# Kernel tuning notes

Measured on AMD Instinct MI355X. Metric: run time of the kernel, lower is better.

Reference implementation:

```python
import jax, jax.numpy as jnp
import numpy as np

B, N, D_IN = 16, 2048, 256
C, H = 32, 64          # num_capsules, dim_capsules
HEADS, KD = 4, 64      # attention heads, key_dim = dim_capsules
ROUTINGS = 3
EPS_SQ = 1e-7
LN_EPS = 1e-3


def squash(v, axis=-1):
    s2 = jnp.sum(jnp.square(v), axis=axis, keepdims=True)
    scale = s2 / (1.0 + s2) / jnp.sqrt(s2 + EPS_SQ)
    return scale * v


def setup_inputs() -> dict:
    key = jax.random.key(0)
    ks = jax.random.split(key, 10)
    # VarianceScaling(scale=2.0, fan_avg, uniform) for W
    fan_avg = (D_IN + H) / 2.0
    limit = float(np.sqrt(3.0 * 2.0 / fan_avg))
    W = jax.random.uniform(ks[0], (C, D_IN, H), minval=-limit, maxval=limit, dtype=jnp.float32)
    b_caps = jnp.zeros((C, H), jnp.float32)
    gamma = jnp.full((1,), 3.0, jnp.float32)
    x = jax.random.normal(ks[1], (B, N, D_IN), dtype=jnp.float32)
    def glorot(k, shape):
        fin, fout = shape[0], int(np.prod(shape[1:]))
        lim = float(np.sqrt(6.0 / (fin + fout)))
        return jax.random.uniform(k, shape, minval=-lim, maxval=lim, dtype=jnp.float32)
    Wq = glorot(ks[2], (H, HEADS, KD)); bq = jnp.zeros((HEADS, KD), jnp.float32)
    Wk = glorot(ks[3], (H, HEADS, KD)); bk = jnp.zeros((HEADS, KD), jnp.float32)
    Wv = glorot(ks[4], (H, HEADS, KD)); bv = jnp.zeros((HEADS, KD), jnp.float32)
    Wo = glorot(ks[5], (HEADS, KD, H)); bo = jnp.zeros((H,), jnp.float32)
    ln_gamma = jnp.ones((H,), jnp.float32)
    ln_beta = jnp.zeros((H,), jnp.float32)
    return dict(x=x, W=W, b_caps=b_caps, gamma=gamma,
                Wq=Wq, bq=bq, Wk=Wk, bk=bk, Wv=Wv, bv=bv, Wo=Wo, bo=bo,
                ln_gamma=ln_gamma, ln_beta=ln_beta)


def dynamic_routing(u_hat):
    # u_hat: [B, N, C, H]
    b = jnp.zeros(u_hat.shape[:3] + (1,), u_hat.dtype)
    v = None
    for i in range(ROUTINGS):
        c = jax.nn.softmax(b, axis=2)                      # [B,N,C,1]
        s = jnp.sum(c * u_hat, axis=1, keepdims=True)      # [B,1,C,H]
        v = squash(s, axis=-1)
        if i < ROUTINGS - 1:
            agreement = jnp.sum(u_hat * v, axis=-1, keepdims=True)
            b = b + agreement
    return jnp.squeeze(v, axis=1)                          # [B,C,H]


def mha_self(xq, Wq, bq, Wk, bk, Wv, bv, Wo, bo):
    # xq: [B, C, H]
    q = jnp.einsum('bch,hnk->bcnk', xq, Wq) + bq
    k = jnp.einsum('bch,hnk->bcnk', xq, Wk) + bk
    v = jnp.einsum('bch,hnk->bcnk', xq, Wv) + bv
    scores = jnp.einsum('bqnd,bknd->bnqk', q, k) / jnp.sqrt(jnp.asarray(KD, xq.dtype))
    attn = jax.nn.softmax(scores, axis=-1)
    ctx = jnp.einsum('bnqk,bknd->bqnd', attn, v)
    return jnp.einsum('bqnd,ndh->bqh', ctx, Wo) + bo


def reference(x, W, b_caps, gamma, Wq, bq, Wk, bk, Wv, bv, Wo, bo, ln_gamma, ln_beta):
    u_hat = jnp.einsum('bnd,cdh->bnch', x, W) + b_caps[None, None]  # [B,N,C,H]
    routed = dynamic_routing(u_hat)                                  # [B,C,H]
    attended = mha_self(routed, Wq, bq, Wk, bk, Wv, bv, Wo, bo)
    y = attended + routed
    mu = jnp.mean(y, axis=-1, keepdims=True)
    var = jnp.mean(jnp.square(y - mu), axis=-1, keepdims=True)
    routed = (y - mu) / jnp.sqrt(var + LN_EPS) * ln_gamma + ln_beta
    return squash(routed, axis=-1) * gamma
```

## Files before the change

### kernel.cpp

```cpp
#include <hip/hip_runtime.h>
#include <hip/hip_cooperative_groups.h>
#include <cstddef>

namespace cg = cooperative_groups;

typedef _Float16 f16;
typedef __attribute__((ext_vector_type(8))) _Float16 f16x8;
typedef __attribute__((ext_vector_type(4))) float f32x4;

namespace {
constexpr int kB = 16;
constexpr int kN = 2048;
constexpr int kD = 256;
constexpr int kC = 32;
constexpr int kH = 64;
constexpr int kHeads = 4;
constexpr int kKD = 64;
constexpr int kChunks = 32;
constexpr int kRows = kN / kChunks;
constexpr int kXJ = 64;

constexpr size_t OFF_XPART = 0;
constexpr size_t OFF_V     = OFF_XPART + 262144;
constexpr size_t OFF_WV    = OFF_V + 32768;
constexpr size_t OFF_BV    = OFF_WV + 131072;
constexpr size_t OFF_Y     = OFF_BV + 512;
constexpr size_t OFF_CS    = OFF_Y + 131072;
constexpr size_t OFF_QKV   = OFF_CS + 512;
constexpr size_t OFF_CTX   = OFF_QKV + 393216;
constexpr size_t OFF_XF16  = OFF_CTX + 524288;
constexpr size_t OFF_WVH   = OFF_XF16 + 4194304;
constexpr size_t OFF_CSP   = OFF_WVH + 65536;
constexpr size_t OFF_YP    = OFF_CSP + 16384;
constexpr size_t WS_NEED_PARTIAL = (OFF_YP + 4194304) * sizeof(float);

struct SMemR {
  f16 xsT[kD][kRows + 8];
  float aL[kRows][kC + 4];
  f16 pT[kC][kRows + 8];
  float csL[8][kC];
  float yL[kD];
  float sL[4][kH];
  float vL[kH];
  float csLs;
};
struct SMemA {
  float rL[kC * kH];
  float qL[kC][kKD];
  float kL[kC][kKD + 1];
  float vL[kC][kKD];
  float sc[kC][kC + 1];
};
struct SMemF {
  float cL[kHeads * kKD];
  float sL[4][kH];
};
union SMemU { SMemR r; SMemA a; SMemF f; };
}


template <int CW, int ACC, int WRV>
__device__ __forceinline__ void sv_tail(const float* __restrict__ W,
                                        const float* __restrict__ b_caps,
                                        SMemR& r, float* __restrict__ v,
                                        float* __restrict__ Wv, f16* __restrict__ wvh,
                                        float* __restrict__ bv, int b, int c, int t) {
  const int w = t >> 6, h = t & 63;
  const float* Wc = W + (size_t)c * kD * kH;
  {
    float acc = 0.f;
#pragma unroll 8
    for (int d = w * 64; d < (w + 1) * 64; ++d)
      acc = fmaf(r.yL[d], Wc[(size_t)d * kH + h], acc);
    r.sL[w][h] = acc;
  }
  __syncthreads();
  if (t < 64) {
    const float bch = b_caps[c * kH + h];
    float s = r.sL[0][h] + r.sL[1][h] + r.sL[2][h] + r.sL[3][h] + r.csLs * bch;
    float s2 = s * s;
#pragma unroll
    for (int off = 32; off; off >>= 1) s2 += __shfl_xor(s2, off, 64);
    const float scale = s2 / (1.f + s2) * rsqrtf(s2 + 1e-7f);
    const float vh = scale * s;
    if (WRV) v[((size_t)b * kC + c) * kH + h] = vh;
    r.vL[h] = vh;
    if (CW) {
      float bvp = bch * vh;
#pragma unroll
      for (int off = 32; off; off >>= 1) bvp += __shfl_xor(bvp, off, 64);
      if (h == 0) bv[b * kC + c] = ACC ? (bv[b * kC + c] + bvp) : bvp;
    }
  }
  __syncthreads();
  if (CW) {
    float acc = 0.f;
    const float* Wrow = Wc + (size_t)t * kH;
#pragma unroll 8
    for (int hh = 0; hh < kH; ++hh) acc = fmaf(Wrow[hh], r.vL[hh], acc);
    const size_t idx = ((size_t)b * kC + c) * kD + t;
    const float nv = ACC ? (Wv[idx] + acc) : acc;
    Wv[idx] = nv;
    wvh[idx] = (f16)nv;
  }
}

__device__ __forceinline__ void route_phase(SMemR& r, const f16x8* __restrict__ af,
                                            const f16* __restrict__ wvh,
                                            const float* __restrict__ bv,
                                            f16* __restrict__ yp, float* __restrict__ csp,
                                            int b, int chunk, int t) {
  const int lane = t & 63, w = t >> 6;
  const int l15 = lane & 15, q = lane >> 4;
  const float bvc = bv[b * kC + (t & 31)];

  f32x4 acc0 = {0.f, 0.f, 0.f, 0.f}, acc1 = {0.f, 0.f, 0.f, 0.f};
  {
    const f16x8* B0 = reinterpret_cast<const f16x8*>(
        wvh + ((size_t)(b * kC + l15)) * kD + q * 8);
    const f16x8* B1 = reinterpret_cast<const f16x8*>(
        wvh + ((size_t)(b * kC + 16 + l15)) * kD + q * 8);
#pragma unroll
    for (int ks = 0; ks < 8; ++ks) {
      acc0 = __builtin_amdgcn_mfma_f32_16x16x32_f16(af[ks], B0[ks * 4], acc0, 0, 0, 0);
      acc1 = __builtin_amdgcn_mfma_f32_16x16x32_f16(af[ks], B1[ks * 4], acc1, 0, 0, 0);
    }
  }
#pragma unroll
  for (int rr = 0; rr < 4; ++rr) {
    r.aL[w * 16 + q * 4 + rr][l15] = acc0[rr];
    r.aL[w * 16 + q * 4 + rr][16 + l15] = acc1[rr];
  }
  __syncthreads();

  const int c = t & 31, sg = t >> 5;
  float csreg = 0.f;
#pragma unroll
  for (int k = 0; k < 8; ++k) {
    const int rr = sg * 8 + k;
    float L = bvc + r.aL[rr][c];
    float m = L;
#pragma unroll
    for (int off = 16; off; off >>= 1) m = fmaxf(m, __shfl_xor(m, off, 64));
    const float e = __expf(L - m);
    float ssum = e;
#pragma unroll
    for (int off = 16; off; off >>= 1) ssum += __shfl_xor(ssum, off, 64);
    const float p = e / ssum;
    r.pT[c][rr] = (f16)p;
    csreg += p;
  }
  r.csL[sg][c] = csreg;
  __syncthreads();

  const int mt2 = w & 1;
  const int ntb = (w >> 1) * 8;
  const f16x8 a0 = *reinterpret_cast<const f16x8*>(&r.pT[mt2 * 16 + l15][q * 8]);
  const f16x8 a1 = *reinterpret_cast<const f16x8*>(&r.pT[mt2 * 16 + l15][32 + q * 8]);
  const int cap = mt2 * 16 + q * 4;
#pragma unroll
  for (int i = 0; i < 8; ++i) {
    const int d0 = (ntb + i) * 16;
    const f16x8 b0 = *reinterpret_cast<const f16x8*>(&r.xsT[d0 + l15][q * 8]);
    const f16x8 b1 = *reinterpret_cast<const f16x8*>(&r.xsT[d0 + l15][32 + q * 8]);
    f32x4 o = {0.f, 0.f, 0.f, 0.f};
    o = __builtin_amdgcn_mfma_f32_16x16x32_f16(a0, b0, o, 0, 0, 0);
    o = __builtin_amdgcn_mfma_f32_16x16x32_f16(a1, b1, o, 0, 0, 0);
    f16* dst = yp + (((size_t)(b * kChunks + chunk)) * kC + cap) * kD + d0 + l15;
#pragma unroll
    for (int rr = 0; rr < 4; ++rr) dst[(size_t)rr * kD] = (f16)o[rr];
  }
  if (t < 32) {
    float s = 0.f;
#pragma unroll
    for (int j = 0; j < 8; ++j) s += r.csL[j][t];
    csp[((size_t)b * kChunks + chunk) * kC + t] = s;
  }
}

__global__ __launch_bounds__(256, 2) void k_fused(
    const float* __restrict__ x, const float* __restrict__ W,
    const float* __restrict__ b_caps, const float* __restrict__ gamma,
    const float* __restrict__ Wq, const float* __restrict__ bq,
    const float* __restrict__ Wk, const float* __restrict__ bk,
    const float* __restrict__ Wvp, const float* __restrict__ bvp,
    const float* __restrict__ Wo, const float* __restrict__ bo,
    const float* __restrict__ ln_g, const float* __restrict__ ln_b,
    float* __restrict__ out, float* __restrict__ ws) {
  float* xpart = ws + OFF_XPART;
  float* v     = ws + OFF_V;
  float* Wv    = ws + OFF_WV;
  float* bv    = ws + OFF_BV;
  float* ctx   = ws + OFF_CTX;
  f16*   wvh   = (f16*)(ws + OFF_WVH);
  float* csp   = ws + OFF_CSP;
  f16*   yp    = (f16*)(ws + OFF_YP);

  const int b = blockIdx.x, chunk = blockIdx.y;
  const int t = threadIdx.x;
  const int lane = t & 63, w = t >> 6;
  const int l15 = lane & 15, q = lane >> 4;
  const int n0 = chunk * kRows;
  const int c = chunk;

  __shared__ __align__(16) SMemU sm;
  cg::grid_group grid = cg::this_grid();

  {
    const float* xc = x + ((size_t)b * kN + n0) * kD + t;
    float s = 0.f;
#pragma unroll 16
    for (int n = 0; n < kRows; ++n) s += xc[(size_t)n * kD];
    xpart[((size_t)b * kChunks + chunk) * kD + t] = s;
  }
  f16x8 af[8];
  {
    const int row = w * 16 + l15;
    const float* xr = x + ((size_t)(b * kN + n0 + row)) * kD + q * 8;
#pragma unroll
    for (int ks = 0; ks < 8; ++ks) {
      const f32x4* p = reinterpret_cast<const f32x4*>(xr + ks * 32);
      const f32x4 lo = p[0], hi = p[1];
      f16x8 a;
      a[0] = (f16)lo[0]; a[1] = (f16)lo[1]; a[2] = (f16)lo[2]; a[3] = (f16)lo[3];
      a[4] = (f16)hi[0]; a[5] = (f16)hi[1]; a[6] = (f16)hi[2]; a[7] = (f16)hi[3];
      af[ks] = a;
      const int dbase = ks * 32 + q * 8;
#pragma unroll
      for (int i = 0; i < 8; ++i) {
        const int ii = (i + 2 * q) & 7;
        sm.r.xsT[dbase + ii][row] = a[ii];
      }
    }
  }
  grid.sync();

  {
    float s = 0.f;
#pragma unroll 8
    for (int ch = 0; ch < kChunks; ++ch)
      s += xpart[((size_t)b * kChunks + ch) * kD + t];
    sm.r.yL[t] = s * (1.f / (float)kC);
    if (t == 0) sm.r.csLs = (float)kN / (float)kC;
  }
  __syncthreads();
  sv_tail<1, 0, 0>(W, b_caps, sm.r, v, Wv, wvh, bv, b, c, t);
  grid.sync();

  route_phase(sm.r, af, wvh, bv, yp, csp, b, chunk, t);
  grid.sync();

  {
    float s = 0.f;
#pragma unroll 8
    for (int ch = 0; ch < kChunks; ++ch)
      s += (float)yp[(((size_t)b * kChunks + ch) * kC + c) * kD + t];
    sm.r.yL[t] = s;
    if (t < 32) {
      float cs_ = csp[((size_t)b * kChunks + t) * kC + c];
#pragma unroll
      for (int off = 16; off; off >>= 1) cs_ += __shfl_xor(cs_, off, 64);
      if (t == 0) sm.r.csLs = cs_;
    }
  }
  __syncthreads();
  sv_tail<1, 1, 0>(W, b_caps, sm.r, v, Wv, wvh, bv, b, c, t);
  grid.sync();

  route_phase(sm.r, af, wvh, bv, yp, csp, b, chunk, t);
  grid.sync();

  {
    float s = 0.f;
#pragma unroll 8
    for (int ch = 0; ch < kChunks; ++ch)
      s += (float)yp[(((size_t)b * kChunks + ch) * kC + c) * kD + t];
    sm.r.yL[t] = s;
    if (t < 32) {
      float cs_ = csp[((size_t)b * kChunks + t) * kC + c];
#pragma unroll
      for (int off = 16; off; off >>= 1) cs_ += __shfl_xor(cs_, off, 64);
      if (t == 0) sm.r.csLs = cs_;
    }
  }
  __syncthreads();
  sv_tail<0, 0, 1>(W, b_caps, sm.r, v, Wv, wvh, bv, b, c, t);
  grid.sync();

  if (chunk < kHeads) {
    const int head = chunk;
    const int kk = t & 63;
#pragma unroll
    for (int i = 0; i < 8; ++i)
      sm.a.rL[t + 256 * i] = v[(size_t)b * kC * kH + t + 256 * i];
    __syncthreads();
    float aq[8], ak[8], av[8];
    const float bbq = bq[head * kKD + kk];
    const float bbk = bk[head * kKD + kk];
    const float bbv = bvp[head * kKD + kk];
#pragma unroll
    for (int i = 0; i < 8; ++i) { aq[i] = bbq; ak[i] = bbk; av[i] = bbv; }
#pragma unroll 4
    for (int hh = 0; hh < kH; ++hh) {
      const size_t widx = ((size_t)hh * kHeads + head) * kKD + kk;
      const float wq = Wq[widx];
      const float wk2 = Wk[widx];
      const float wv2 = Wvp[widx];
#pragma unroll
      for (int i = 0; i < 8; ++i) {
        const float rv = sm.a.rL[(w + 4 * i) * kH + hh];
        aq[i] = fmaf(rv, wq, aq[i]);
        ak[i] = fmaf(rv, wk2, ak[i]);
        av[i] = fmaf(rv, wv2, av[i]);
      }
    }
#pragma unroll
    for (int i = 0; i < 8; ++i) {
      const int cc = w + 4 * i;
      sm.a.qL[cc][kk] = aq[i];
      sm.a.kL[cc][kk] = ak[i];
      sm.a.vL[cc][kk] = av[i];
    }
    __syncthreads();
#pragma unroll
    for (int i = 0; i < 4; ++i) {
      const int e = t + 256 * i, qc = e >> 5, kc2 = e & 31;
      float s = 0.f;
#pragma unroll 8
      for (int d = 0; d < kKD; ++d) s = fmaf(sm.a.qL[qc][d], sm.a.kL[kc2][d], s);
      sm.a.sc[qc][kc2] = s * 0.125f;
    }
    __syncthreads();
    if (t < kC) {
      float m = -1e30f;
#pragma unroll
      for (int kc2 = 0; kc2 < kC; ++kc2) m = fmaxf(m, sm.a.sc[t][kc2]);
      float ssum = 0.f;
#pragma unroll
      for (int kc2 = 0; kc2 < kC; ++kc2) {
        const float e2 = __expf(sm.a.sc[t][kc2] - m);
        sm.a.sc[t][kc2] = e2;
        ssum += e2;
      }
      const float inv = 1.f / ssum;
#pragma unroll
      for (int kc2 = 0; kc2 < kC; ++kc2) sm.a.sc[t][kc2] *= inv;
    }
    __syncthreads();
#pragma unroll
    for (int i = 0; i < 8; ++i) {
      const int e = t + 256 * i, qc = e >> 6, d = e & 63;
      float s = 0.f;
#pragma unroll 8
      for (int kc2 = 0; kc2 < kC; ++kc2) s = fmaf(sm.a.sc[qc][kc2], sm.a.vL[kc2][d], s);
      ctx[(((size_t)b * kC + qc) * kHeads + head) * kKD + d] = s;
    }
  }
  grid.sync();

  {
    const int bc = b * kC + chunk;
    const int h = t & 63;
    sm.f.cL[t] = ctx[(size_t)bc * (kHeads * kKD) + t];
    __syncthreads();
    float acc = 0.f;
#pragma unroll 8
    for (int nd = w * 64; nd < (w + 1) * 64; ++nd)
      acc = fmaf(sm.f.cL[nd], Wo[(size_t)nd * kH + h], acc);
    sm.f.sL[w][h] = acc;
    __syncthreads();
    if (t < 64) {
      const float yv = sm.f.sL[0][h] + sm.f.sL[1][h] + sm.f.sL[2][h] + sm.f.sL[3][h] +
                       bo[h] + v[(size_t)bc * kH + h];
      float mu = yv;
#pragma unroll
      for (int off = 32; off; off >>= 1) mu += __shfl_xor(mu, off, 64);
      mu *= (1.f / (float)kH);
      const float dv = yv - mu;
      float var = dv * dv;
#pragma unroll
      for (int off = 32; off; off >>= 1) var += __shfl_xor(var, off, 64);
      var *= (1.f / (float)kH);
      const float nrm = dv * rsqrtf(var + 1e-3f) * ln_g[h] + ln_b[h];
      float s2 = nrm * nrm;
#pragma unroll
      for (int off = 32; off; off >>= 1) s2 += __shfl_xor(s2, off, 64);
      const float scale = s2 / (1.f + s2) * rsqrtf(s2 + 1e-7f);
      out[(size_t)bc * kH + h] = scale * nrm * gamma[0];
    }
  }
}


__global__ __launch_bounds__(256) void k_xpart(const float* __restrict__ x,
                                               float* __restrict__ xpart,
                                               f16* __restrict__ xh) {
  const int b = blockIdx.x, j = blockIdx.y, d = threadIdx.x;
  const size_t base = ((size_t)b * kN + (size_t)j * 32) * kD + d;
  const float* xp = x + base;
  f16* xo = xh + base;
  float s = 0.f;
#pragma unroll
  for (int n = 0; n < 32; ++n) {
    const float v = xp[(size_t)n * kD];
    s += v;
    xo[(size_t)n * kD] = (f16)v;
  }
  xpart[((size_t)b * kXJ + j) * kD + d] = s;
}

__global__ __launch_bounds__(256) void k_sv(
    const float* __restrict__ W, const float* __restrict__ b_caps,
    const float* __restrict__ xpart, const float* __restrict__ y,
    const float* __restrict__ csum, const f16* __restrict__ ypart,
    const float* __restrict__ cspart, float* __restrict__ v,
    float* __restrict__ Wv, f16* __restrict__ Wvh, float* __restrict__ bv,
    const int mode, const int computeWv, const int accWv, const int npart) {
  const int bc = blockIdx.x, b = bc >> 5, c = bc & 31;
  const int t = threadIdx.x;
  const int w = t >> 6, h = t & 63;
  __shared__ float yL[kD];
  __shared__ float sL[4][kH];
  __shared__ float vL[kH];
  __shared__ float csLs;

  if (mode == 0) {
    float s = 0.f;
#pragma unroll 8
    for (int j = 0; j < kXJ; ++j) s += xpart[((size_t)b * kXJ + j) * kD + t];
    yL[t] = s * (1.f / (float)kC);
    if (t == 0) csLs = (float)kN / (float)kC;
  } else if (npart > 0) {
    float s = 0.f;
#pragma unroll 8
    for (int ch = 0; ch < kChunks; ++ch)
      s += (float)ypart[(((size_t)b * kChunks + ch) * kC + c) * kD + t];
    yL[t] = s;
    if (t < 32) {
      float cs_ = cspart[((size_t)b * kChunks + t) * kC + c];
#pragma unroll
      for (int off = 16; off; off >>= 1) cs_ += __shfl_xor(cs_, off, 64);
      if (t == 0) csLs = cs_;
    }
  } else {
    yL[t] = y[(size_t)bc * kD + t];
    if (t == 0) csLs = csum[bc];
  }
  __syncthreads();

  const float* Wc = W + (size_t)c * kD * kH;
  {
    float acc = 0.f;
#pragma unroll 8
    for (int d = w * 64; d < (w + 1) * 64; ++d)
      acc = fmaf(yL[d], Wc[(size_t)d * kH + h], acc);
    sL[w][h] = acc;
  }
  __syncthreads();

  if (t < 64) {
    const float bch = b_caps[c * kH + h];
    float s = sL[0][h] + sL[1][h] + sL[2][h] + sL[3][h] + csLs * bch;
    float s2 = s * s;
#pragma unroll
    for (int off = 32; off; off >>= 1) s2 += __shfl_xor(s2, off, 64);
    const float scale = s2 / (1.f + s2) * rsqrtf(s2 + 1e-7f);
    const float vh = scale * s;
    v[(size_t)bc * kH + h] = vh;
    vL[h] = vh;
    if (computeWv) {
      float bvp = bch * vh;
#pragma unroll
      for (int off = 32; off; off >>= 1) bvp += __shfl_xor(bvp, off, 64);
      if (h == 0) bv[bc] = accWv ? (bv[bc] + bvp) : bvp;
    }
  }
  __syncthreads();
  if (computeWv) {
    float acc = 0.f;
    const float* Wrow = Wc + (size_t)t * kH;
#pragma unroll 8
    for (int hh = 0; hh < kH; ++hh) acc = fmaf(Wrow[hh], vL[hh], acc);
    const size_t idx = (size_t)bc * kD + t;
    const float nv = accWv ? (Wv[idx] + acc) : acc;
    Wv[idx] = nv;
    Wvh[idx] = (f16)nv;
  }
}

__global__ __launch_bounds__(256) void k_route(
    const f16* __restrict__ xh, const f16* __restrict__ Wvh,
    const float* __restrict__ bv, float* __restrict__ y,
    float* __restrict__ csum, f16* __restrict__ ypart,
    float* __restrict__ cspart, const int usePart) {
  const int b = blockIdx.x, chunk = blockIdx.y;
  const int t = threadIdx.x;
  const int lane = t & 63, w = t >> 6;
  const int l15 = lane & 15, q = lane >> 4;

  __shared__ __align__(16) f16 xsT[kD][kRows + 8];
  __shared__ float aL[kRows][kC + 4];
  __shared__ __align__(16) f16 pT[kC][kRows + 8];
  __shared__ float csL[8][kC];

  const int n0 = chunk * kRows;
  const float bvc = bv[b * kC + (t & 31)];

  f32x4 acc0 = {0.f, 0.f, 0.f, 0.f}, acc1 = {0.f, 0.f, 0.f, 0.f};
  {
    const int row = w * 16 + l15;
    const f16x8* Ar = reinterpret_cast<const f16x8*>(
        xh + ((size_t)(b * kN + n0 + row)) * kD + q * 8);
    const f16x8* B0 = reinterpret_cast<const f16x8*>(
        Wvh + ((size_t)(b * kC + l15)) * kD + q * 8);
    const f16x8* B1 = reinterpret_cast<const f16x8*>(
        Wvh + ((size_t)(b * kC + 16 + l15)) * kD + q * 8);
#pragma unroll
    for (int ks = 0; ks < 8; ++ks) {
      f16x8 af = Ar[ks * 4];
      acc0 = __builtin_amdgcn_mfma_f32_16x16x32_f16(af, B0[ks * 4], acc0, 0, 0, 0);
      acc1 = __builtin_amdgcn_mfma_f32_16x16x32_f16(af, B1[ks * 4], acc1, 0, 0, 0);
      const int dbase = ks * 32 + q * 8;
#pragma unroll
      for (int i = 0; i < 8; ++i) {
        const int ii = (i + 2 * q) & 7;
        xsT[dbase + ii][row] = af[ii];
      }
    }
  }
#pragma unroll
  for (int r = 0; r < 4; ++r) {
    aL[w * 16 + q * 4 + r][l15] = acc0[r];
    aL[w * 16 + q * 4 + r][16 + l15] = acc1[r];
  }
  __syncthreads();

  const int c = t & 31, sg = t >> 5;
  float csreg = 0.f;
#pragma unroll
  for (int k = 0; k < 8; ++k) {
    const int r = sg * 8 + k;
    float L = bvc + aL[r][c];
    float m = L;
#pragma unroll
    for (int off = 16; off; off >>= 1) m = fmaxf(m, __shfl_xor(m, off, 64));
    const float e = __expf(L - m);
    float ssum = e;
#pragma unroll
    for (int off = 16; off; off >>= 1) ssum += __shfl_xor(ssum, off, 64);
    const float p = e / ssum;
    pT[c][r] = (f16)p;
    csreg += p;
  }
  csL[sg][c] = csreg;
  __syncthreads();

  const int mt2 = w & 1;
  const int ntb = (w >> 1) * 8;
  const f16x8 a0 = *reinterpret_cast<const f16x8*>(&pT[mt2 * 16 + l15][q * 8]);
  const f16x8 a1 = *reinterpret_cast<const f16x8*>(&pT[mt2 * 16 + l15][32 + q * 8]);
  const int cap = mt2 * 16 + q * 4;
#pragma unroll
  for (int i = 0; i < 8; ++i) {
    const int d0 = (ntb + i) * 16;
    const f16x8 b0 = *reinterpret_cast<const f16x8*>(&xsT[d0 + l15][q * 8]);
    const f16x8 b1 = *reinterpret_cast<const f16x8*>(&xsT[d0 + l15][32 + q * 8]);
    f32x4 o = {0.f, 0.f, 0.f, 0.f};
    o = __builtin_amdgcn_mfma_f32_16x16x32_f16(a0, b0, o, 0, 0, 0);
    o = __builtin_amdgcn_mfma_f32_16x16x32_f16(a1, b1, o, 0, 0, 0);
    if (usePart) {
      f16* dst = ypart + (((size_t)(b * kChunks + chunk)) * kC + cap) * kD + d0 + l15;
#pragma unroll
      for (int r = 0; r < 4; ++r) dst[(size_t)r * kD] = (f16)o[r];
    } else {
      float* dst = y + ((size_t)(b * kC + cap)) * kD + d0 + l15;
#pragma unroll
      for (int r = 0; r < 4; ++r) atomicAdd(dst + (size_t)r * kD, o[r]);
    }
  }
  if (t < 32) {
    float s = 0.f;
#pragma unroll
    for (int j = 0; j < 8; ++j) s += csL[j][t];
    if (usePart) cspart[((size_t)b * kChunks + chunk) * kC + t] = s;
    else atomicAdd(csum + b * kC + t, s);
  }
}

__global__ __launch_bounds__(256) void k_attn(
    const float* __restrict__ routed,
    const float* __restrict__ Wq, const float* __restrict__ bq,
    const float* __restrict__ Wk, const float* __restrict__ bk,
    const float* __restrict__ Wvp, const float* __restrict__ bvp,
    float* __restrict__ ctx) {
  const int b = blockIdx.x, head = blockIdx.y, t = threadIdx.x;
  const int kk = t & 63, w = t >> 6;
  __shared__ float rL[kC * kH];
  __shared__ float qL[kC][kKD];
  __shared__ float kL[kC][kKD + 1];
  __shared__ float vL[kC][kKD];
  __shared__ float sc[kC][kC + 1];
#pragma unroll
  for (int i = 0; i < 8; ++i) rL[t + 256 * i] = routed[(size_t)b * kC * kH + t + 256 * i];
  __syncthreads();
  float aq[8], ak[8], av[8];
  const float bbq = bq[head * kKD + kk];
  const float bbk = bk[head * kKD + kk];
  const float bbv = bvp[head * kKD + kk];
#pragma unroll
  for (int i = 0; i < 8; ++i) { aq[i] = bbq; ak[i] = bbk; av[i] = bbv; }
#pragma unroll 4
  for (int hh = 0; hh < kH; ++hh) {
    const size_t widx = ((size_t)hh * kHeads + head) * kKD + kk;
    const float wq = Wq[widx];
    const float wk2 = Wk[widx];
    const float wv2 = Wvp[widx];
#pragma unroll
    for (int i = 0; i < 8; ++i) {
      const float r = rL[(w + 4 * i) * kH + hh];
      aq[i] = fmaf(r, wq, aq[i]);
      ak[i] = fmaf(r, wk2, ak[i]);
      av[i] = fmaf(r, wv2, av[i]);
    }
  }
#pragma unroll
  for (int i = 0; i < 8; ++i) {
    const int cc = w + 4 * i;
    qL[cc][kk] = aq[i];
    kL[cc][kk] = ak[i];
    vL[cc][kk] = av[i];
  }
  __syncthreads();
#pragma unroll
  for (int i = 0; i < 4; ++i) {
    const int e = t + 256 * i, qc = e >> 5, kc2 = e & 31;
    float s = 0.f;
#pragma unroll 8
    for (int d = 0; d < kKD; ++d) s = fmaf(qL[qc][d], kL[kc2][d], s);
    sc[qc][kc2] = s * 0.125f;
  }
  __syncthreads();
  if (t < kC) {
    float m = -1e30f;
#pragma unroll
    for (int kc2 = 0; kc2 < kC; ++kc2) m = fmaxf(m, sc[t][kc2]);
    float ssum = 0.f;
#pragma unroll
    for (int kc2 = 0; kc2 < kC; ++kc2) {
      const float e2 = __expf(sc[t][kc2] - m);
      sc[t][kc2] = e2;
      ssum += e2;
    }
    const float inv = 1.f / ssum;
#pragma unroll
    for (int kc2 = 0; kc2 < kC; ++kc2) sc[t][kc2] *= inv;
  }
  __syncthreads();
#pragma unroll
  for (int i = 0; i < 8; ++i) {
    const int e = t + 256 * i, qc = e >> 6, d = e & 63;
    float s = 0.f;
#pragma unroll 8
    for (int kc2 = 0; kc2 < kC; ++kc2) s = fmaf(sc[qc][kc2], vL[kc2][d], s);
    ctx[(((size_t)b * kC + qc) * kHeads + head) * kKD + d] = s;
  }
}

__global__ __launch_bounds__(256) void k_final(
    const float* __restrict__ ctx, const float* __restrict__ Wo,
    const float* __restrict__ bo, const float* __restrict__ routed,
    const float* __restrict__ ln_g, const float* __restrict__ ln_b,
    const float* __restrict__ gamma, float* __restrict__ out) {
  const int bc = blockIdx.x, t = threadIdx.x;
  const int w = t >> 6, h = t & 63;
  __shared__ float cL[kHeads * kKD];
  __shared__ float sL[4][kH];
  cL[t] = ctx[(size_t)bc * (kHeads * kKD) + t];
  __syncthreads();
  float acc = 0.f;
#pragma unroll 8
  for (int nd = w * 64; nd < (w + 1) * 64; ++nd)
    acc = fmaf(cL[nd], Wo[(size_t)nd * kH + h], acc);
  sL[w][h] = acc;
  __syncthreads();
  if (t < 64) {
    const float yv = sL[0][h] + sL[1][h] + sL[2][h] + sL[3][h] + bo[h] +
                     routed[(size_t)bc * kH + h];
    float mu = yv;
#pragma unroll
    for (int off = 32; off; off >>= 1) mu += __shfl_xor(mu, off, 64);
    mu *= (1.f / (float)kH);
    const float dv = yv - mu;
    float var = dv * dv;
#pragma unroll
    for (int off = 32; off; off >>= 1) var += __shfl_xor(var, off, 64);
    var *= (1.f / (float)kH);
    const float nrm = dv * rsqrtf(var + 1e-3f) * ln_g[h] + ln_b[h];
    float s2 = nrm * nrm;
#pragma unroll
    for (int off = 32; off; off >>= 1) s2 += __shfl_xor(s2, off, 64);
    const float scale = s2 / (1.f + s2) * rsqrtf(s2 + 1e-7f);
    out[(size_t)bc * kH + h] = scale * nrm * gamma[0];
  }
}

extern "C" void kernel_launch(void* const* d_in, const int* in_sizes, int n_in,
                              void* d_out, int out_size, void* d_ws, size_t ws_size,
                              hipStream_t stream) {
  (void)in_sizes; (void)n_in; (void)out_size;
  const float* x      = (const float*)d_in[0];
  const float* W      = (const float*)d_in[1];
  const float* b_caps = (const float*)d_in[2];
  const float* gamma  = (const float*)d_in[3];
  const float* Wq     = (const float*)d_in[4];
  const float* bq     = (const float*)d_in[5];
  const float* Wk     = (const float*)d_in[6];
  const float* bk     = (const float*)d_in[7];
  const float* Wv_in  = (const float*)d_in[8];
  const float* bv_in  = (const float*)d_in[9];
  const float* Wo     = (const float*)d_in[10];
  const float* bo     = (const float*)d_in[11];
  const float* ln_g   = (const float*)d_in[12];
  const float* ln_b   = (const float*)d_in[13];
  float* out = (float*)d_out;
  float* ws  = (float*)d_ws;

  static int s_coop = -1;
  if (s_coop < 0) {
    int dev = 0;
    hipGetDevice(&dev);
    hipDeviceProp_t prop{};
    hipGetDeviceProperties(&prop, dev);
    int occ = 0;
    hipError_t e = hipOccupancyMaxActiveBlocksPerMultiprocessor(&occ, k_fused, 256, 0);
    s_coop = (e == hipSuccess && prop.cooperativeLaunch &&
              (long long)occ * prop.multiProcessorCount >= (long long)kB * kChunks)
                 ? 1 : 0;
  }

  if (s_coop && ws_size >= WS_NEED_PARTIAL) {
    void* args[] = {(void*)&x,     (void*)&W,     (void*)&b_caps, (void*)&gamma,
                    (void*)&Wq,    (void*)&bq,    (void*)&Wk,     (void*)&bk,
                    (void*)&Wv_in, (void*)&bv_in, (void*)&Wo,     (void*)&bo,
                    (void*)&ln_g,  (void*)&ln_b,  (void*)&out,    (void*)&ws};
    hipLaunchCooperativeKernel((void*)k_fused, dim3(kB, kChunks), dim3(256, 1, 1),
                               args, 0, stream);
    return;
  }

  float* xpart = ws + OFF_XPART;
  float* v     = ws + OFF_V;
  float* Wv    = ws + OFF_WV;
  float* bv    = ws + OFF_BV;
  float* y     = ws + OFF_Y;
  float* cs    = ws + OFF_CS;
  float* ctx   = ws + OFF_CTX;
  f16*   xf16  = (f16*)(ws + OFF_XF16);
  f16*   wvh   = (f16*)(ws + OFF_WVH);
  float* csp   = ws + OFF_CSP;
  f16*   yp    = (f16*)(ws + OFF_YP);

  const int usePart = (ws_size >= WS_NEED_PARTIAL) ? 1 : 0;

  k_xpart<<<dim3(kB, kXJ), 256, 0, stream>>>(x, xpart, xf16);
  k_sv<<<kB * kC, 256, 0, stream>>>(W, b_caps, xpart, y, cs, yp, csp, v, Wv, wvh, bv,
                                    0, 1, 0, 0);
  if (!usePart) {
    hipMemsetAsync(y, 0, (size_t)kB * kC * kD * sizeof(float), stream);
    hipMemsetAsync(cs, 0, (size_t)kB * kC * sizeof(float), stream);
  }
  k_route<<<dim3(kB, kChunks), 256, 0, stream>>>(xf16, wvh, bv, y, cs, yp, csp, usePart);
  k_sv<<<kB * kC, 256, 0, stream>>>(W, b_caps, xpart, y, cs, yp, csp, v, Wv, wvh, bv,
                                    1, 1, 1, usePart ? kChunks : 0);
  if (!usePart) {
    hipMemsetAsync(y, 0, (size_t)kB * kC * kD * sizeof(float), stream);
    hipMemsetAsync(cs, 0, (size_t)kB * kC * sizeof(float), stream);
  }
  k_route<<<dim3(kB, kChunks), 256, 0, stream>>>(xf16, wvh, bv, y, cs, yp, csp, usePart);
  k_sv<<<kB * kC, 256, 0, stream>>>(W, b_caps, xpart, y, cs, yp, csp, v, Wv, wvh, bv,
                                    1, 0, 0, usePart ? kChunks : 0);
  k_attn<<<dim3(kB, kHeads), 256, 0, stream>>>(v, Wq, bq, Wk, bk, Wv_in, bv_in, ctx);
  k_final<<<kB * kC, 256, 0, stream>>>(ctx, Wo, bo, v, ln_g, ln_b, gamma, out);
}
```

Baseline: 174.4 us.

## Replace cooperative grid syncs with per-batch atomic barriers over normal launch

Swaps the cooperative launch and its grid-wide syncs for a per-batch counter barrier held in workspace, so each batch's 32 blocks wait only on one another instead of the entire grid. A memset before each launch clears the counters, and the kernel now goes out through an ordinary launch. The intent is to cut the cost of grid barriers and the cooperative-launch overhead, and to let different batches move ahead independently. The risk is that co-residency is no longer guaranteed, so correctness relies on the occupancy check and a bounded spin guard, and the extra memset adds a small launch.

```diff
diff --git a/kernel.cpp b/kernel.cpp
--- a/kernel.cpp
+++ b/kernel.cpp
@@ -1,8 +1,5 @@
 #include <hip/hip_runtime.h>
-#include <hip/hip_cooperative_groups.h>
 #include <cstddef>
-
-namespace cg = cooperative_groups;
 
 typedef _Float16 f16;
 typedef __attribute__((ext_vector_type(8))) _Float16 f16x8;
@@ -26,8 +23,8 @@
 constexpr size_t OFF_BV    = OFF_WV + 131072;
 constexpr size_t OFF_Y     = OFF_BV + 512;
 constexpr size_t OFF_CS    = OFF_Y + 131072;
-constexpr size_t OFF_QKV   = OFF_CS + 512;
-constexpr size_t OFF_CTX   = OFF_QKV + 393216;
+constexpr size_t OFF_BAR   = OFF_CS + 512;
+constexpr size_t OFF_CTX   = OFF_BAR + 393216;
 constexpr size_t OFF_XF16  = OFF_CTX + 524288;
 constexpr size_t OFF_WVH   = OFF_XF16 + 4194304;
 constexpr size_t OFF_CSP   = OFF_WVH + 65536;
@@ -58,6 +55,20 @@
 union SMemU { SMemR r; SMemA a; SMemF f; };
 }
 
+__device__ __forceinline__ void bbar(int* __restrict__ bar, int b, int target) {
+  __syncthreads();
+  if (threadIdx.x == 0) {
+    __hip_atomic_fetch_add(&bar[b * 16], 1, __ATOMIC_RELEASE,
+                           __HIP_MEMORY_SCOPE_AGENT);
+    int guard = 0;
+    while (__hip_atomic_load(&bar[b * 16], __ATOMIC_ACQUIRE,
+                             __HIP_MEMORY_SCOPE_AGENT) < target) {
+      __builtin_amdgcn_s_sleep(1);
+      if (++guard > (1 << 22)) break;
+    }
+  }
+  __syncthreads();
+}
 
 template <int CW, int ACC, int WRV>
 __device__ __forceinline__ void sv_tail(const float* __restrict__ W,
@@ -178,7 +189,7 @@
   }
 }
 
-__global__ __launch_bounds__(256, 2) void k_fused(
+__global__ __launch_bounds__(256, 2) void k_all(
     const float* __restrict__ x, const float* __restrict__ W,
     const float* __restrict__ b_caps, const float* __restrict__ gamma,
     const float* __restrict__ Wq, const float* __restrict__ bq,
@@ -191,6 +202,7 @@
   float* v     = ws + OFF_V;
   float* Wv    = ws + OFF_WV;
   float* bv    = ws + OFF_BV;
+  int*   bar   = (int*)(ws + OFF_BAR);
   float* ctx   = ws + OFF_CTX;
   f16*   wvh   = (f16*)(ws + OFF_WVH);
   float* csp   = ws + OFF_CSP;
@@ -204,7 +216,6 @@
   const int c = chunk;
 
   __shared__ __align__(16) SMemU sm;
-  cg::grid_group grid = cg::this_grid();
 
   {
     const float* xc = x + ((size_t)b * kN + n0) * kD + t;
@@ -233,7 +244,7 @@
       }
     }
   }
-  grid.sync();
+  bbar(bar, b, 32 * 1);
 
   {
     float s = 0.f;
@@ -245,10 +256,10 @@
   }
   __syncthreads();
   sv_tail<1, 0, 0>(W, b_caps, sm.r, v, Wv, wvh, bv, b, c, t);
-  grid.sync();
+  bbar(bar, b, 32 * 2);
 
   route_phase(sm.r, af, wvh, bv, yp, csp, b, chunk, t);
-  grid.sync();
+  bbar(bar, b, 32 * 3);
 
   {
     float s = 0.f;
@@ -265,10 +276,10 @@
   }
   __syncthreads();
   sv_tail<1, 1, 0>(W, b_caps, sm.r, v, Wv, wvh, bv, b, c, t);
-  grid.sync();
+  bbar(bar, b, 32 * 4);
 
   route_phase(sm.r, af, wvh, bv, yp, csp, b, chunk, t);
-  grid.sync();
+  bbar(bar, b, 32 * 5);
 
   {
     float s = 0.f;
@@ -285,7 +296,7 @@
   }
   __syncthreads();
   sv_tail<0, 0, 1>(W, b_caps, sm.r, v, Wv, wvh, bv, b, c, t);
-  grid.sync();
+  bbar(bar, b, 32 * 6);
 
   if (chunk < kHeads) {
     const int head = chunk;
@@ -356,7 +367,7 @@
       ctx[(((size_t)b * kC + qc) * kHeads + head) * kKD + d] = s;
     }
   }
-  grid.sync();
+  bbar(bar, b, 32 * 7);
 
   {
     const int bc = b * kC + chunk;
@@ -725,26 +736,24 @@
   float* out = (float*)d_out;
   float* ws  = (float*)d_ws;
 
-  static int s_coop = -1;
-  if (s_coop < 0) {
+  static int s_ok = -1;
+  if (s_ok < 0) {
     int dev = 0;
     hipGetDevice(&dev);
     hipDeviceProp_t prop{};
     hipGetDeviceProperties(&prop, dev);
     int occ = 0;
-    hipError_t e = hipOccupancyMaxActiveBlocksPerMultiprocessor(&occ, k_fused, 256, 0);
-    s_coop = (e == hipSuccess && prop.cooperativeLaunch &&
-              (long long)occ * prop.multiProcessorCount >= (long long)kB * kChunks)
-                 ? 1 : 0;
-  }
-
-  if (s_coop && ws_size >= WS_NEED_PARTIAL) {
-    void* args[] = {(void*)&x,     (void*)&W,     (void*)&b_caps, (void*)&gamma,
-                    (void*)&Wq,    (void*)&bq,    (void*)&Wk,     (void*)&bk,
-                    (void*)&Wv_in, (void*)&bv_in, (void*)&Wo,     (void*)&bo,
-                    (void*)&ln_g,  (void*)&ln_b,  (void*)&out,    (void*)&ws};
-    hipLaunchCooperativeKernel((void*)k_fused, dim3(kB, kChunks), dim3(256, 1, 1),
-                               args, 0, stream);
+    hipError_t e = hipOccupancyMaxActiveBlocksPerMultiprocessor(&occ, k_all, 256, 0);
+    s_ok = (e == hipSuccess &&
+            (long long)occ * prop.multiProcessorCount >= (long long)kB * kChunks)
+               ? 1 : 0;
+  }
+
+  if (s_ok && ws_size >= WS_NEED_PARTIAL) {
+    hipMemsetAsync((void*)(ws + OFF_BAR), 0, kB * 16 * sizeof(int), stream);
+    k_all<<<dim3(kB, kChunks), 256, 0, stream>>>(
+        x, W, b_caps, gamma, Wq, bq, Wk, bk, Wv_in, bv_in, Wo, bo, ln_g, ln_b,
+        out, ws);
     return;
   }
 
```

Result: no change. 175.3 us (+0.6%).
